# Performance work log

Hardware: AMD Instinct MI355X
Metric: run time of the kernel (lower is better)

The kernel has to match this reference:

```python
import jax, jax.numpy as jnp
import numpy as np

GRID_SIZE = 5
SPLINE_ORDER = 3
GRID_LO, GRID_HI = -1.0, 1.0
N_HEADS = 8
N_PATCHES = 256
EPS = 1e-5


def make_grid(in_features):
    h = (GRID_HI - GRID_LO) / GRID_SIZE
    g = jnp.arange(-SPLINE_ORDER, GRID_SIZE + SPLINE_ORDER + 1, dtype=jnp.float32) * h + GRID_LO
    return jnp.broadcast_to(g, (in_features, g.shape[0]))  # (in, G+2k+1)


def b_splines(x, grid):
    # x: (M, in) -> bases (M, in, G+k) via Cox-de Boor recursion
    xe = x[..., None]
    bases = ((xe >= grid[:, :-1]) & (xe < grid[:, 1:])).astype(x.dtype)
    for j in range(1, SPLINE_ORDER + 1):
        left = (xe - grid[:, :-(j + 1)]) / (grid[:, j:-1] - grid[:, :-(j + 1)]) * bases[..., :-1]
        right = (grid[:, j + 1:] - xe) / (grid[:, j + 1:] - grid[:, 1:-j]) * bases[..., 1:]
        bases = left + right
    return bases


def kan_linear(x, base_w, spline_w, scaler, grid):
    # x: (..., in); base_w: (out, in); spline_w: (out, in, G+k); scaler: (out, in)
    in_dim = x.shape[-1]
    out_dim = base_w.shape[0]
    xf = x.reshape(-1, in_dim)
    base = jax.nn.silu(xf) @ base_w.T
    sw = (spline_w * scaler[..., None]).reshape(out_dim, -1)  # scaled_spline_weight
    spl = b_splines(xf, grid).reshape(xf.shape[0], -1) @ sw.T
    return (base + spl).reshape(*x.shape[:-1], out_dim)


def layer_norm(x, g, b):
    m = jnp.mean(x, axis=-1, keepdims=True)
    v = jnp.var(x, axis=-1, keepdims=True)
    return (x - m) * jax.lax.rsqrt(v + EPS) * g + b


def mha(h, in_w, in_b, out_w, out_b):
    B, S, D = h.shape
    hd = D // N_HEADS
    qkv = h @ in_w.T + in_b
    q, k, v = jnp.split(qkv, 3, axis=-1)
    sh = lambda t: t.reshape(B, S, N_HEADS, hd).transpose(0, 2, 1, 3)
    q, k, v = sh(q), sh(k), sh(v)
    att = jax.nn.softmax(jnp.einsum('bhqd,bhkd->bhqk', q, k) / jnp.sqrt(jnp.float32(hd)), axis=-1)
    o = jnp.einsum('bhqk,bhkd->bhqd', att, v).transpose(0, 2, 1, 3).reshape(B, S, D)
    return o @ out_w.T + out_b


def setup_inputs() -> dict:
    key = jax.random.key(0)
    ks = jax.random.split(key, 20)
    B, L, E, D, H, OUT = 64, 64, 384, 512, 512, 256
    NB = GRID_SIZE + SPLINE_ORDER  # num spline basis = 8
    inp = {
        'x': jax.random.normal(ks[0], (B, 1 + L, E), jnp.float32),
        'ids_restore': jax.random.randint(ks[1], (B, N_PATCHES), 0, N_PATCHES, jnp.int64),
        'dec_w': jax.random.normal(ks[2], (D, E), jnp.float32) * 0.02,
        'dec_b': jnp.zeros((D,), jnp.float32),
        'mask_token': jax.random.normal(ks[3], (1, 1, D), jnp.float32) * 0.02,
        'pos_embed': jax.random.normal(ks[4], (1, 1025, D), jnp.float32) * 0.02,
        'ln1_g': jnp.ones((D,), jnp.float32),
        'ln1_b': jnp.zeros((D,), jnp.float32),
        'in_w': jax.random.normal(ks[5], (3 * D, D), jnp.float32) * 0.02,
        'in_b': jnp.zeros((3 * D,), jnp.float32),
        'out_w': jax.random.normal(ks[6], (D, D), jnp.float32) * 0.02,
        'out_b': jnp.zeros((D,), jnp.float32),
        'ln2_g': jnp.ones((D,), jnp.float32),
        'ln2_b': jnp.zeros((D,), jnp.float32),
        'k1_base': jax.random.normal(ks[7], (H, D), jnp.float32) * 0.05,
        'k1_spline': jax.random.normal(ks[8], (H, D, NB), jnp.float32) * 0.05,
        'k1_scaler': jnp.ones((H, D), jnp.float32),
        'k2_base': jax.random.normal(ks[9], (OUT, H), jnp.float32) * 0.05,
        'k2_spline': jax.random.normal(ks[10], (OUT, H, NB), jnp.float32) * 0.05,
        'k2_scaler': jnp.ones((OUT, H), jnp.float32),
    }
    return inp


def reference(x, ids_restore, dec_w, dec_b, mask_token, pos_embed, ln1_g, ln1_b,
              in_w, in_b, out_w, out_b, ln2_g, ln2_b,
              k1_base, k1_spline, k1_scaler, k2_base, k2_spline, k2_scaler):
    B = x.shape[0]
    N = ids_restore.shape[1]
    D = dec_w.shape[0]
    # 1. linear projection
    x = x @ dec_w.T + dec_b  # (B, 1+L, D)
    # 2. splice mask tokens + restore order + pos embed
    n_mask = N + 1 - x.shape[1]
    mask_tokens = jnp.broadcast_to(mask_token, (B, n_mask, D))
    x_ = jnp.concatenate([x[:, 1:, :], mask_tokens], axis=1)  # (B, N, D)
    x_ = jnp.take_along_axis(x_, ids_restore[:, :, None], axis=1)
    x = jnp.concatenate([x[:, :1, :], x_], axis=1)  # (B, N+1, D)
    x = x + pos_embed[:, :N + 1, :]
    # 3. pre-norm MHA + residual
    h = layer_norm(x, ln1_g, ln1_b)
    x = x + mha(h, in_w, in_b, out_w, out_b)
    # 4. KAN head
    x = layer_norm(x, ln2_g, ln2_b)
    x = kan_linear(x, k1_base, k1_spline, k1_scaler, make_grid(k1_base.shape[1]))
    x = kan_linear(x, k2_base, k2_spline, k2_scaler, make_grid(k2_base.shape[1]))
    return x[:, 1:, :]
```

## Files before the change

### kernel.cpp

```cpp
#include <hip/hip_runtime.h>
#include <hip/hip_bf16.h>
#include <math.h>

#define DMODEL 512
#define SEQ    257
#define BATCH  64
#define ROWS   (BATCH * SEQ)
#define ROWSP  16512
#define HCHUNK 8224

typedef unsigned short ushortT;
typedef __attribute__((ext_vector_type(8))) __bf16 bf16x8;
typedef __attribute__((ext_vector_type(4))) float f32x4;

__device__ __forceinline__ ushortT f2bf(float v) {
    __hip_bfloat16 t = __float2bfloat16(v);
    return *(ushortT*)&t;
}
__device__ __forceinline__ float bf2f(ushortT u) {
    return __bfloat162float(*(__hip_bfloat16*)&u);
}

__device__ __forceinline__ void gl16(const ushortT* g, ushortT* l) {
    __builtin_amdgcn_global_load_lds(
        (const __attribute__((address_space(1))) void*)g,
        (__attribute__((address_space(3))) void*)l, 16, 0, 0);
}

__device__ __forceinline__ void bspline8(float x, float bas[8]) {
    const float k6 = 1.0f / 6.0f;
    float t = (x + 2.2f) * 2.5f;
    float fm = floorf(t);
    int m = (int)fm;
    float u = t - fm;
    float u2 = u * u, u3 = u2 * u;
    float omu = 1.0f - u;
    float p0 = u3 * k6;
    float p1 = (-3.0f * u3 + 3.0f * u2 + 3.0f * u + 1.0f) * k6;
    float p2 = (3.0f * u3 - 6.0f * u2 + 4.0f) * k6;
    float p3 = omu * omu * omu * k6;
#pragma unroll
    for (int q = 0; q < 8; ++q) {
        int d = m - q;
        float v = (d == 0) ? p0 : (d == 1) ? p1 : (d == 2) ? p2 : (d == 3) ? p3 : 0.0f;
        bas[q] = v;
    }
}

template<int MODE>
__global__ __launch_bounds__(256) void gemm_t(
    const ushortT* __restrict__ A, const ushortT* __restrict__ B,
    const float* __restrict__ bias, const float* __restrict__ R,
    void* __restrict__ Cv, int N, int K, int Mreal, int rowoff, int Ks) {
    __shared__ __align__(16) ushortT As[128 * 32];
    __shared__ __align__(16) ushortT Bs[128 * 32];
    const int tid = threadIdx.x;
    const int wave = tid >> 6, lane = tid & 63;
    const int nwg = gridDim.x * gridDim.y;
    const int lin = blockIdx.y * gridDim.x + blockIdx.x;
    const int xcd = lin & 7, sidx = lin >> 3;
    const int qn = nwg >> 3, rn = nwg & 7;
    const int nlin = (xcd < rn ? xcd * (qn + 1) : rn * (qn + 1) + (xcd - rn) * qn) + sidx;
    const int bm = (nlin / gridDim.x) * 128, bn = (nlin % gridDim.x) * 128;
    const int wm = (wave >> 1) * 64, wn = (wave & 1) * 64;
    const int srow = tid >> 2;
    const int scol = (tid & 3) * 8;
    const int mrow = lane & 15;
    const int kq = (lane >> 4) * 8;
    f32x4 acc[4][4];
#pragma unroll
    for (int i = 0; i < 4; ++i)
#pragma unroll
        for (int j = 0; j < 4; ++j) acc[i][j] = (f32x4){0.f, 0.f, 0.f, 0.f};

    int ar0 = bm + srow;      if (ar0 > Mreal - 1) ar0 = Mreal - 1;
    int ar1 = bm + srow + 64; if (ar1 > Mreal - 1) ar1 = Mreal - 1;
    const ushortT* Ab0 = A + (size_t)ar0 * K + scol;
    const ushortT* Ab1 = A + (size_t)ar1 * K + scol;
    const ushortT* Bb  = B + (size_t)(bn + srow) * K + scol;
    ushortT* AsW = As + wave * 512;
    ushortT* BsW = Bs + wave * 512;
    const int kb = blockIdx.z * Ks;
    const int ke = kb + Ks;
    for (int k0 = kb; k0 < ke; k0 += 32) {
        __syncthreads();
        gl16(Ab0 + k0, AsW);
        gl16(Ab1 + k0, AsW + 2048);
        gl16(Bb + k0, BsW);
        gl16(Bb + k0 + (size_t)64 * K, BsW + 2048);
        __syncthreads();
        bf16x8 af[4], bf[4];
#pragma unroll
        for (int i = 0; i < 4; ++i) af[i] = *(const bf16x8*)&As[(wm + i * 16 + mrow) * 32 + kq];
#pragma unroll
        for (int j = 0; j < 4; ++j) bf[j] = *(const bf16x8*)&Bs[(wn + j * 16 + mrow) * 32 + kq];
#pragma unroll
        for (int i = 0; i < 4; ++i)
#pragma unroll
            for (int j = 0; j < 4; ++j)
                acc[i][j] = __builtin_amdgcn_mfma_f32_16x16x32_bf16(af[i], bf[j], acc[i][j], 0, 0, 0);
    }
    const int r0q = (lane >> 4) * 4;
    const int cn = lane & 15;
#pragma unroll
    for (int i = 0; i < 4; ++i) {
#pragma unroll
        for (int j = 0; j < 4; ++j) {
            int col = bn + wn + j * 16 + cn;
            float bv = (MODE <= 1) ? bias[col] : 0.0f;
#pragma unroll
            for (int r = 0; r < 4; ++r) {
                int row = bm + wm + i * 16 + r0q + r;
                float v = acc[i][j][r] + bv;
                if (MODE == 1) {
                    if (row < Mreal)
                        ((__hip_bfloat16*)Cv)[(size_t)row * N + col] = __float2bfloat16(v);
                } else if (MODE == 0) {
                    if (row < Mreal) {
                        size_t idx = (size_t)row * N + col;
                        if (R) v += R[idx];
                        ((float*)Cv)[idx] = v;
                    }
                } else if (MODE == 3) {
                    if (row < Mreal)
                        atomicAdd(&((float*)Cv)[(size_t)row * N + col], v);
                } else {
                    if (row < Mreal) {
                        int grow = rowoff + row;
                        int bb = grow / SEQ;
                        int pp = grow - bb * SEQ;
                        if (pp > 0)
                            atomicAdd(&((float*)Cv)[((size_t)(bb * 256 + pp - 1)) * 256 + col], v);
                    }
                }
            }
        }
    }
}

__global__ __launch_bounds__(256) void attn_mf2(const ushortT* __restrict__ qkvb,
                                                __hip_bfloat16* __restrict__ o) {
    __shared__ __align__(16) ushortT KV[20992];
    __shared__ __align__(16) ushortT Sc[64 * 296];
    __shared__ float Linv[64];
    const int tid = threadIdx.x;
    const int wave = tid >> 6, lane = tid & 63;
    const int l15 = lane & 15;
    const int quad = lane >> 4;
    const int lin = blockIdx.y * gridDim.x + blockIdx.x;
    const int w = (lin & 7) * 320 + (lin >> 3);
    const int q0 = (w % 5) * 64;
    const int bh = w / 5;
    const int h = bh & 7, b = bh >> 3;
    const size_t base = (size_t)(b * SEQ) * 1536;

    for (int g = tid; g < 272 * 8; g += 256) {
        int k = g >> 3;
        int d0 = (g & 7) * 8;
        int4 v;
        if (k < SEQ) v = *(const int4*)&qkvb[base + (size_t)k * 1536 + 512 + h * 64 + d0];
        else v = (int4){0, 0, 0, 0};
        *(int4*)&KV[k * 72 + d0] = v;
    }
    int q = q0 + wave * 16 + l15;
    if (q > SEQ - 1) q = SEQ - 1;
    bf16x8 qf[2];
#pragma unroll
    for (int c = 0; c < 2; ++c) {
        union { bf16x8 v8; ushortT u[8]; } r;
        r.v8 = *(const bf16x8*)&qkvb[base + (size_t)q * 1536 + h * 64 + quad * 8 + c * 32];
#pragma unroll
        for (int i = 0; i < 8; ++i)
            r.u[i] = f2bf(bf2f(r.u[i]) * 0.125f);
        qf[c] = r.v8;
    }
    __syncthreads();

    __builtin_amdgcn_s_setprio(1);
    for (int kt = 0; kt < 17; ++kt) {
        f32x4 sacc = (f32x4){0.f, 0.f, 0.f, 0.f};
#pragma unroll
        for (int c = 0; c < 2; ++c) {
            bf16x8 kf = *(const bf16x8*)&KV[(kt * 16 + l15) * 72 + c * 32 + quad * 8];
            sacc = __builtin_amdgcn_mfma_f32_16x16x32_bf16(qf[c], kf, sacc, 0, 0, 0);
        }
#pragma unroll
        for (int r = 0; r < 4; ++r)
            Sc[(wave * 16 + quad * 4 + r) * 296 + kt * 16 + l15] = f2bf(sacc[r]);
    }
    __builtin_amdgcn_s_setprio(0);
    __syncthreads();

    for (int g = tid; g < 288 * 8; g += 256) {
        int key = g >> 3;
        int d0 = (g & 7) * 8;
        ushortT tmp[8];
        if (key < SEQ) {
            int4 v = *(const int4*)&qkvb[base + (size_t)key * 1536 + 1024 + h * 64 + d0];
            *(int4*)tmp = v;
        } else {
#pragma unroll
            for (int i = 0; i < 8; ++i) tmp[i] = 0;
        }
        int sk = key ^ d0;
#pragma unroll
        for (int i = 0; i < 8; ++i) KV[(d0 + i) * 328 + sk] = tmp[i];
    }
    {
        int row = tid >> 2;
        int stripe = tid & 3;
        ushortT* sr = &Sc[row * 296];
        ushortT NEG = f2bf(-1e30f);
        for (int c = SEQ + stripe; c < 288; c += 4) sr[c] = NEG;
        float m = -1e30f;
#pragma unroll
        for (int it = 0; it < 9; ++it) {
            union { bf16x8 v8; ushortT u[8]; } rr;
            rr.v8 = *(const bf16x8*)&sr[stripe * 8 + it * 32];
#pragma unroll
            for (int j = 0; j < 8; ++j) m = fmaxf(m, bf2f(rr.u[j]));
        }
        m = fmaxf(m, __shfl_xor(m, 1, 64));
        m = fmaxf(m, __shfl_xor(m, 2, 64));
        float l = 0.f;
#pragma unroll
        for (int it = 0; it < 9; ++it) {
            union { bf16x8 v8; ushortT u[8]; } rr;
            ushortT* p = &sr[stripe * 8 + it * 32];
            rr.v8 = *(const bf16x8*)p;
#pragma unroll
            for (int j = 0; j < 8; ++j) {
                float e = __expf(bf2f(rr.u[j]) - m);
                l += e;
                rr.u[j] = f2bf(e);
            }
            *(bf16x8*)p = rr.v8;
        }
        l += __shfl_xor(l, 1, 64);
        l += __shfl_xor(l, 2, 64);
        if (stripe == 0) Linv[row] = 1.0f / l;
    }
    __syncthreads();

    f32x4 oacc[4];
#pragma unroll
    for (int nf = 0; nf < 4; ++nf) oacc[nf] = (f32x4){0.f, 0.f, 0.f, 0.f};
    __builtin_amdgcn_s_setprio(1);
    for (int kc = 0; kc < 9; ++kc) {
        bf16x8 pf = *(const bf16x8*)&Sc[(wave * 16 + l15) * 296 + kc * 32 + quad * 8];
#pragma unroll
        for (int nf = 0; nf < 4; ++nf) {
            int d = nf * 16 + l15;
            int mask = ((d >> 3) & 7) * 8;
            bf16x8 vf = *(const bf16x8*)&KV[d * 328 + ((kc * 32 + quad * 8) ^ mask)];
            oacc[nf] = __builtin_amdgcn_mfma_f32_16x16x32_bf16(pf, vf, oacc[nf], 0, 0, 0);
        }
    }
    __builtin_amdgcn_s_setprio(0);
#pragma unroll
    for (int nf = 0; nf < 4; ++nf) {
#pragma unroll
        for (int r = 0; r < 4; ++r) {
            int rr = quad * 4 + r;
            int qq = q0 + wave * 16 + rr;
            if (qq < SEQ)
                o[(size_t)(b * SEQ + qq) * DMODEL + h * 64 + nf * 16 + l15] =
                    __float2bfloat16(oacc[nf][r] * Linv[wave * 16 + rr]);
        }
    }
}

__global__ __launch_bounds__(256) void cvt_bf16_k(const float* __restrict__ s,
                                                  __hip_bfloat16* __restrict__ d, int n) {
    int i = blockIdx.x * 256 + threadIdx.x;
    if (i < n) d[i] = __float2bfloat16(s[i]);
}

__global__ __launch_bounds__(256) void asm_ln1(const float* __restrict__ x1,
        const int* __restrict__ ids, const float* __restrict__ mask_tok,
        const float* __restrict__ pos, const float* __restrict__ g,
        const float* __restrict__ bt, float* __restrict__ xres,
        __hip_bfloat16* __restrict__ y) {
    int row = blockIdx.x;
    int t = threadIdx.x;
    __shared__ float sbuf[256];
    int b = row / SEQ, p = row - b * SEQ;
    const float* srcrow;
    if (p == 0) {
        srcrow = x1 + (size_t)(b * 65) * DMODEL;
    } else {
        int i = ids[b * 256 + p - 1];
        srcrow = (i < 64) ? (x1 + (size_t)(b * 65 + 1 + i) * DMODEL) : mask_tok;
    }
    const float* posr = pos + (size_t)p * DMODEL;
    float a0 = srcrow[t] + posr[t];
    float a1 = srcrow[t + 256] + posr[t + 256];
    float* xr = xres + (size_t)row * DMODEL;
    xr[t] = a0;
    xr[t + 256] = a1;
    sbuf[t] = a0 + a1;
    __syncthreads();
    for (int s = 128; s > 0; s >>= 1) { if (t < s) sbuf[t] += sbuf[t + s]; __syncthreads(); }
    float mean = sbuf[0] * (1.0f / DMODEL);
    __syncthreads();
    float d0 = a0 - mean, d1 = a1 - mean;
    sbuf[t] = d0 * d0 + d1 * d1;
    __syncthreads();
    for (int s = 128; s > 0; s >>= 1) { if (t < s) sbuf[t] += sbuf[t + s]; __syncthreads(); }
    float inv = rsqrtf(sbuf[0] * (1.0f / DMODEL) + 1e-5f);
    __hip_bfloat16* yr = y + (size_t)row * DMODEL;
    yr[t]       = __float2bfloat16(d0 * inv * g[t]       + bt[t]);
    yr[t + 256] = __float2bfloat16(d1 * inv * g[t + 256] + bt[t + 256]);
}

__global__ __launch_bounds__(256) void buildw9p(const float* base, const float* spline,
                                                const float* scaler, ushortT* W9, int total) {
    int gid = blockIdx.x * 256 + threadIdx.x;
    if (gid >= total) return;
    int f = gid & 511;
    int o = gid >> 9;
    size_t w = (size_t)o * 4608;
    W9[w + f] = f2bf(base[gid]);
    float sc = scaler[gid];
#pragma unroll
    for (int q = 0; q < 8; ++q)
        W9[w + (size_t)(1 + q) * 512 + f] = f2bf(spline[(size_t)gid * 8 + q] * sc);
}

template<int DOLN>
__global__ __launch_bounds__(256) void expand9p(const float* __restrict__ src,
        const float* __restrict__ g, const float* __restrict__ bt,
        ushortT* __restrict__ E9, int row0, int nrows) {
    const int w = threadIdx.x >> 6;
    const int lane = threadIdx.x & 63;
    const int r = blockIdx.x * 4 + w;
    if (r >= nrows) return;
    const float* xr = src + (size_t)(row0 + r) * DMODEL + lane * 8;
    float v[8];
    *(float4*)&v[0] = *(const float4*)&xr[0];
    *(float4*)&v[4] = *(const float4*)&xr[4];
    if (DOLN) {
        float s = 0.f;
#pragma unroll
        for (int j = 0; j < 8; ++j) s += v[j];
#pragma unroll
        for (int off = 1; off < 64; off <<= 1) s += __shfl_xor(s, off, 64);
        float mean = s * (1.0f / DMODEL);
        float vs = 0.f;
#pragma unroll
        for (int j = 0; j < 8; ++j) { v[j] -= mean; vs += v[j] * v[j]; }
#pragma unroll
        for (int off = 1; off < 64; off <<= 1) vs += __shfl_xor(vs, off, 64);
        float inv = rsqrtf(vs * (1.0f / DMODEL) + 1e-5f);
        float gw[8], bw[8];
        *(float4*)&gw[0] = *(const float4*)&g[lane * 8];
        *(float4*)&gw[4] = *(const float4*)&g[lane * 8 + 4];
        *(float4*)&bw[0] = *(const float4*)&bt[lane * 8];
        *(float4*)&bw[4] = *(const float4*)&bt[lane * 8 + 4];
#pragma unroll
        for (int j = 0; j < 8; ++j) v[j] = v[j] * inv * gw[j] + bw[j];
    }
    ushortT pl[9][8];
#pragma unroll
    for (int j = 0; j < 8; ++j) {
        float x = v[j];
        pl[0][j] = f2bf(x / (1.0f + __expf(-x)));
        float bas[8];
        bspline8(x, bas);
#pragma unroll
        for (int q = 0; q < 8; ++q) pl[1 + q][j] = f2bf(bas[q]);
    }
    ushortT* e = E9 + (size_t)r * 4608 + lane * 8;
#pragma unroll
    for (int pp = 0; pp < 9; ++pp) *(int4*)&e[(size_t)pp * 512] = *(int4*)pl[pp];
}

__global__ void zero_k(float* p, int n) {
    int i = blockIdx.x * 256 + threadIdx.x;
    if (i < n) p[i] = 0.0f;
}
__global__ void fill_out_k(float* o, int n) {
    int i = blockIdx.x * 256 + threadIdx.x;
    if (i < n) o[i] = 333.0f;
}
__global__ void diag_host_k(float* o, float val) {
    if (threadIdx.x == 0 && blockIdx.x == 0) o[0] = val;
}

extern "C" void kernel_launch(void* const* d_in, const int* in_sizes, int n_in,
                              void* d_out, int out_size, void* d_ws, size_t ws_size,
                              hipStream_t stream) {
    const float* x      = (const float*)d_in[0];
    const int*   ids    = (const int*)d_in[1];
    const float* dec_w  = (const float*)d_in[2];
    const float* dec_b  = (const float*)d_in[3];
    const float* mask_t = (const float*)d_in[4];
    const float* pos    = (const float*)d_in[5];
    const float* ln1_g  = (const float*)d_in[6];
    const float* ln1_b  = (const float*)d_in[7];
    const float* in_w   = (const float*)d_in[8];
    const float* in_b   = (const float*)d_in[9];
    const float* out_w  = (const float*)d_in[10];
    const float* out_b  = (const float*)d_in[11];
    const float* ln2_g  = (const float*)d_in[12];
    const float* ln2_b  = (const float*)d_in[13];
    const float* k1_base = (const float*)d_in[14];
    const float* k1_spl  = (const float*)d_in[15];
    const float* k1_sc   = (const float*)d_in[16];
    const float* k2_base = (const float*)d_in[17];
    const float* k2_spl  = (const float*)d_in[18];
    const float* k2_sc   = (const float*)d_in[19];
    float* out = (float*)d_out;

    static const int exp_sizes[20] = {
        1597440, 16384, 196608, 512, 512, 524800, 512, 512,
        786432, 1536, 262144, 512, 512, 512,
        262144, 2097152, 262144, 131072, 1048576, 131072
    };
    int bad = -1;
    if (n_in != 20) bad = 55;
    else {
        for (int i = 0; i < 20; ++i)
            if (in_sizes[i] != exp_sizes[i]) { bad = i; break; }
        if (bad < 0 && out_size != 4194304) bad = 56;
    }
    if (bad >= 0) {
        fill_out_k<<<(out_size + 255) / 256, 256, 0, stream>>>(out, out_size);
        diag_host_k<<<1, 64, 0, stream>>>(out, ldexpf(1.0f, 30 + bad));
        return;
    }

    float* ws = (float*)d_ws;
    ushortT* W9a   = (ushortT*)(ws);
    ushortT* W9b   = (ushortT*)(ws + 1179648);
    float*   zeros = ws + 1769472;
    float*   xres  = ws + 1769984;
    __hip_bfloat16* hbufb = (__hip_bfloat16*)(ws + 10224128);
    ushortT* qkvb  = (ushortT*)(ws + 14451200);
    float*   x1    = ws + 14451200;
    ushortT* xbf   = (ushortT*)(ws + 16613888);
    float*   kan1o = ws + 10224128;
    ushortT* E9    = (ushortT*)(ws + 18645504);
    ushortT* dec_wb = (ushortT*)(ws + 37593600);
    ushortT* in_wb  = (ushortT*)(ws + 37691904);
    ushortT* out_wb = (ushortT*)(ws + 38085120);

    zero_k<<<2, 256, 0, stream>>>(zeros, 512);
    cvt_bf16_k<<<(1597440 + 255) / 256, 256, 0, stream>>>(x, (__hip_bfloat16*)xbf, 1597440);
    cvt_bf16_k<<<(196608 + 255) / 256, 256, 0, stream>>>(dec_w, (__hip_bfloat16*)dec_wb, 196608);
    cvt_bf16_k<<<(786432 + 255) / 256, 256, 0, stream>>>(in_w, (__hip_bfloat16*)in_wb, 786432);
    cvt_bf16_k<<<(262144 + 255) / 256, 256, 0, stream>>>(out_w, (__hip_bfloat16*)out_wb, 262144);
    buildw9p<<<(262144 + 255) / 256, 256, 0, stream>>>(k1_base, k1_spl, k1_sc, W9a, 262144);
    buildw9p<<<(131072 + 255) / 256, 256, 0, stream>>>(k2_base, k2_spl, k2_sc, W9b, 131072);

    gemm_t<0><<<dim3(4, 33), 256, 0, stream>>>(xbf, dec_wb, dec_b, nullptr, x1,
                                               512, 384, 4224, 0, 384);
    asm_ln1<<<ROWS, 256, 0, stream>>>(x1, ids, mask_t, pos, ln1_g, ln1_b, xres, hbufb);
    gemm_t<1><<<dim3(12, 129), 256, 0, stream>>>((const ushortT*)hbufb, in_wb, in_b, nullptr,
                                                 qkvb, 1536, 512, 16512, 0, 512);
    attn_mf2<<<dim3(5, BATCH * 8), 256, 0, stream>>>(qkvb, hbufb);
    gemm_t<0><<<dim3(4, 129), 256, 0, stream>>>((const ushortT*)hbufb, out_wb, out_b, xres,
                                                xres, 512, 512, 16512, 0, 512);

    zero_k<<<(ROWS * 512 + 255) / 256, 256, 0, stream>>>(kan1o, ROWS * 512);
    zero_k<<<(4194304 + 255) / 256, 256, 0, stream>>>(out, 4194304);

    for (int c = 0; c < 2; ++c) {
        int r0 = c * HCHUNK;
        expand9p<1><<<(HCHUNK + 3) / 4, 256, 0, stream>>>(xres, ln2_g, ln2_b, E9, r0, HCHUNK);
        gemm_t<3><<<dim3(4, 65, 2), 256, 0, stream>>>(E9, W9a, zeros, nullptr,
                                                      kan1o + (size_t)r0 * 512,
                                                      512, 4608, HCHUNK, 0, 2304);
    }
    for (int c = 0; c < 2; ++c) {
        int r0 = c * HCHUNK;
        expand9p<0><<<(HCHUNK + 3) / 4, 256, 0, stream>>>(kan1o, ln2_g, ln2_b, E9, r0, HCHUNK);
        gemm_t<4><<<dim3(2, 65, 4), 256, 0, stream>>>(E9, W9b, zeros, nullptr,
                                                      out, 256, 4608, HCHUNK, r0, 1152);
    }
    (void)ws_size;
}
```

Baseline: 775.0 us.

## Triple-buffer LDS tiles in GEMM to overlap global loads with MFMA

Replaces the single-buffered LDS staging in the templated GEMM with a three-stage ring buffer. Tiles are prefetched two K-steps ahead using direct global-to-LDS loads, and manual vmcnt waits plus one barrier per iteration replace the two __syncthreads per step. The goal is to hide global memory latency behind MFMA work and cut barrier overhead. In exchange, LDS use per block triples, which may lower occupancy, and the hand-written waitcnt logic makes correctness depend on the exact number of outstanding loads.

```diff
diff --git a/kernel.cpp b/kernel.cpp
--- a/kernel.cpp
+++ b/kernel.cpp
@@ -52,8 +52,8 @@
     const ushortT* __restrict__ A, const ushortT* __restrict__ B,
     const float* __restrict__ bias, const float* __restrict__ R,
     void* __restrict__ Cv, int N, int K, int Mreal, int rowoff, int Ks) {
-    __shared__ __align__(16) ushortT As[128 * 32];
-    __shared__ __align__(16) ushortT Bs[128 * 32];
+    __shared__ __align__(16) ushortT As[3][4096];
+    __shared__ __align__(16) ushortT Bs[3][4096];
     const int tid = threadIdx.x;
     const int wave = tid >> 6, lane = tid & 63;
     const int nwg = gridDim.x * gridDim.y;
@@ -78,27 +78,61 @@
     const ushortT* Ab0 = A + (size_t)ar0 * K + scol;
     const ushortT* Ab1 = A + (size_t)ar1 * K + scol;
     const ushortT* Bb  = B + (size_t)(bn + srow) * K + scol;
-    ushortT* AsW = As + wave * 512;
-    ushortT* BsW = Bs + wave * 512;
     const int kb = blockIdx.z * Ks;
-    const int ke = kb + Ks;
-    for (int k0 = kb; k0 < ke; k0 += 32) {
-        __syncthreads();
-        gl16(Ab0 + k0, AsW);
-        gl16(Ab1 + k0, AsW + 2048);
-        gl16(Bb + k0, BsW);
-        gl16(Bb + k0 + (size_t)64 * K, BsW + 2048);
-        __syncthreads();
-        bf16x8 af[4], bf[4];
-#pragma unroll
-        for (int i = 0; i < 4; ++i) af[i] = *(const bf16x8*)&As[(wm + i * 16 + mrow) * 32 + kq];
-#pragma unroll
-        for (int j = 0; j < 4; ++j) bf[j] = *(const bf16x8*)&Bs[(wn + j * 16 + mrow) * 32 + kq];
+    const int nt = Ks >> 5;
+
+    ushortT *pa0 = As[0], *pa1 = As[1], *pa2 = As[2];
+    ushortT *pb0 = Bs[0], *pb1 = Bs[1], *pb2 = Bs[2];
+    const int woff = wave * 512;
+
+    {
+        gl16(Ab0 + kb, pa0 + woff);
+        gl16(Ab1 + kb, pa0 + woff + 2048);
+        gl16(Bb + kb, pb0 + woff);
+        gl16(Bb + kb + (size_t)64 * K, pb0 + woff + 2048);
+        if (nt > 1) {
+            const int k1 = kb + 32;
+            gl16(Ab0 + k1, pa1 + woff);
+            gl16(Ab1 + k1, pa1 + woff + 2048);
+            gl16(Bb + k1, pb1 + woff);
+            gl16(Bb + k1 + (size_t)64 * K, pb1 + woff + 2048);
+        }
+    }
+    if (nt > 1) { asm volatile("s_waitcnt vmcnt(4)" ::: "memory"); }
+    else        { asm volatile("s_waitcnt vmcnt(0)" ::: "memory"); }
+    __builtin_amdgcn_sched_barrier(0);
+    __builtin_amdgcn_s_barrier();
+    __builtin_amdgcn_sched_barrier(0);
+
+    for (int t = 0; t < nt; ++t) {
+        if (t + 2 < nt) {
+            const int k2 = kb + (t + 2) * 32;
+            gl16(Ab0 + k2, pa2 + woff);
+            gl16(Ab1 + k2, pa2 + woff + 2048);
+            gl16(Bb + k2, pb2 + woff);
+            gl16(Bb + k2 + (size_t)64 * K, pb2 + woff + 2048);
+        }
+        bf16x8 af[4], bfr[4];
 #pragma unroll
         for (int i = 0; i < 4; ++i)
+            af[i] = *(const bf16x8*)&pa0[(wm + i * 16 + mrow) * 32 + kq];
+#pragma unroll
+        for (int j = 0; j < 4; ++j)
+            bfr[j] = *(const bf16x8*)&pb0[(wn + j * 16 + mrow) * 32 + kq];
+#pragma unroll
+        for (int i = 0; i < 4; ++i)
 #pragma unroll
             for (int j = 0; j < 4; ++j)
-                acc[i][j] = __builtin_amdgcn_mfma_f32_16x16x32_bf16(af[i], bf[j], acc[i][j], 0, 0, 0);
+                acc[i][j] = __builtin_amdgcn_mfma_f32_16x16x32_bf16(af[i], bfr[j], acc[i][j], 0, 0, 0);
+        if (t + 1 < nt) {
+            if (t + 2 < nt) { asm volatile("s_waitcnt vmcnt(4)" ::: "memory"); }
+            else            { asm volatile("s_waitcnt vmcnt(0)" ::: "memory"); }
+            __builtin_amdgcn_sched_barrier(0);
+            __builtin_amdgcn_s_barrier();
+            __builtin_amdgcn_sched_barrier(0);
+        }
+        ushortT* tA = pa0; pa0 = pa1; pa1 = pa2; pa2 = tA;
+        ushortT* tB = pb0; pb0 = pb1; pb1 = pb2; pb2 = tB;
     }
     const int r0q = (lane >> 4) * 4;
     const int cn = lane & 15;
```

Result: no change. 765.3 us (-1.3%).
